# Kernel tuning notes

Hardware: AMD Instinct MI355X
Metric: run time of the kernel (lower is better)

Reference implementation:

```python
import jax, jax.numpy as jnp
import numpy as np

C = 1.2            # PoincareBall curvature (learnable in torch, init value used)
SQC = C ** 0.5
MIN_NORM = 1e-15
BALL_EPS = 4e-3    # geoopt float32 projx eps

def _artanh(x):
    return jnp.arctanh(jnp.clip(x, -1.0 + 1e-7, 1.0 - 1e-7))

def _tanh(x):
    return jnp.tanh(jnp.clip(x, -15.0, 15.0))

def _norm(x):
    return jnp.maximum(jnp.linalg.norm(x, axis=-1, keepdims=True), MIN_NORM)

def p_projx(x):
    n = _norm(x)
    maxnorm = (1.0 - BALL_EPS) / SQC
    return jnp.where(n > maxnorm, x / n * maxnorm, x)

def p_expmap0(u):
    n = _norm(u)
    return p_projx(_tanh(SQC * n) * u / (SQC * n))

def p_logmap0(y):
    n = _norm(y)
    return _artanh(SQC * n) * y / (SQC * n)

def p_mobius_add(x, y):
    x2 = jnp.sum(x * x, -1, keepdims=True)
    y2 = jnp.sum(y * y, -1, keepdims=True)
    xy = jnp.sum(x * y, -1, keepdims=True)
    num = (1 + 2 * C * xy + C * y2) * x + (1 - C * x2) * y
    den = 1 + 2 * C * xy + C * C * x2 * y2
    return num / jnp.maximum(den, MIN_NORM)

def p_mobius_matvec(W, x):
    xn = _norm(x)
    mx = x @ W.T
    mxn = _norm(mx)
    res = _tanh(mxn / xn * _artanh(SQC * xn)) * mx / (mxn * SQC)
    zero = jnp.all(mx == 0, axis=-1, keepdims=True)
    return p_projx(jnp.where(zero, jnp.zeros_like(res), res))

def p_mobius_scalar_mul(r, x):
    n = _norm(x)
    return p_projx(_tanh(r * _artanh(SQC * n)) * x / (n * SQC))

def p_linear(x, W, b):
    # Manifold_Linear on PoincareBall: mobius matvec + mobius bias add + projx
    mv = p_mobius_matvec(W, x)
    return p_projx(p_mobius_add(mv, p_expmap0(b)))

def e_linear(x, W, b):
    return x @ W.T + b

def mob_relu(x):
    # Mob_Act: logmap0 -> act -> expmap0 (with projection)
    return p_expmap0(jax.nn.relu(p_logmap0(x)))


def setup_inputs() -> dict:
    key = jax.random.key(0)
    ks = jax.random.split(key, 26)
    g = lambda i, shape, s: (jax.random.normal(ks[i], shape, jnp.float32) * s)
    d = {
        'x':   g(0, (1024, 32, 128), 1.0),
        'We1': g(1, (80, 32), 0.1),   'be1': g(2, (80,), 0.05),
        'We2': g(3, (104, 80), 0.1),  'be2': g(4, (104,), 0.05),
        'We3': g(5, (128, 104), 0.1), 'be3': g(6, (128,), 0.05),
        'Wh1': g(7, (80, 32), 0.1),   'bh1': g(8, (80,), 0.05),
        'Wh2': g(9, (104, 80), 0.1),  'bh2': g(10, (104,), 0.05),
        'Wh3': g(11, (128, 104), 0.1),'bh3': g(12, (128,), 0.05),
        'Wae': g(13, (128, 128), 0.1),'bae': g(14, (128,), 0.05),
        'Wah': g(15, (128, 128), 0.1),'bah': g(16, (128,), 0.05),
        'Wte': g(17, (1, 128), 0.1),  'bte': g(18, (1,), 0.05),
        'Wth': g(19, (1, 128), 0.1),  'bth': g(20, (1,), 0.05),
        'Wf1': g(21, (10, 256), 0.1), 'bf1': g(22, (10,), 0.05),
        'Wf2': g(23, (10, 10), 0.1),  'bf2': g(24, (10,), 0.05),
    }
    return d


def reference(x, We1, be1, We2, be2, We3, be3,
              Wh1, bh1, Wh2, bh2, Wh3, bh3,
              Wae, bae, Wah, bah, Wte, bte, Wth, bth,
              Wf1, bf1, Wf2, bf2):
    xs = jnp.transpose(x, (0, 2, 1))  # (B, S, C_in)

    # --- Euclidean branch: expmap0 = identity; Manifold_Linear = plain linear ---
    xe = xs
    xe = e_linear(xe, We1, be1); xe = jax.nn.relu(xe)
    xe = e_linear(xe, We2, be2); xe = jax.nn.relu(xe)
    xe = e_linear(xe, We3, be3)
    out_e = jax.nn.relu(xe)               # extra self.act for Euclidean manifolds

    # --- Poincare branch ---
    xh = p_expmap0(xs)
    xh = p_linear(xh, Wh1, bh1); xh = mob_relu(xh)
    xh = p_linear(xh, Wh2, bh2); xh = mob_relu(xh)
    out_h = p_linear(xh, Wh3, bh3)        # (B, S, part_dim)

    # --- cross-manifold attention in tangent space at origin ---
    tan_e = e_linear(out_e, Wae, bae)                    # Euclidean logmap0 = id
    tan_h = p_logmap0(p_linear(out_h, Wah, bah))
    mu = 0.5 * (tan_e + tan_h)
    a_e = e_linear(tan_e - mu, Wte, bte)  # (B, S, 1)
    a_h = e_linear(tan_h - mu, Wth, bth)
    w = jax.nn.softmax(jnp.stack([a_e, a_h], axis=0), axis=0)
    proc_e = w[0] * out_e                                # Euclidean mobius scalar mul
    proc_h = p_mobius_scalar_mul(w[1], out_h)

    # --- pool over constituents in tangent space, concat, classify ---
    o_e = jnp.mean(proc_e, axis=1)                       # Euclidean logmap0 = id
    o_h = jnp.mean(p_logmap0(proc_h), axis=1)
    o = jnp.concatenate([o_e, o_h], axis=-1)             # (B, 2*part_dim)
    o = jax.nn.relu(e_linear(o, Wf1, bf1))
    return e_linear(o, Wf2, bf2)
```

## Files before the change

kernel.cpp:

```cpp
#include <hip/hip_runtime.h>
#include <math.h>

constexpr float CC   = 1.2f;
constexpr float SQC  = 1.09544511501033215f;
constexpr float MAXN = (1.0f - 4e-3f) / SQC;
constexpr float MINN = 1e-15f;

constexpr int WTH1 = 0;
constexpr int WTH2 = 4096;
constexpr int WTH3 = 14336;
constexpr int WTAH = 27648;
constexpr int WTE1 = 44032;
constexpr int WTE2 = 48128;
constexpr int WTE3 = 58368;
constexpr int EB1  = 71680;
constexpr int EB2  = 71808;
constexpr int EB3  = 71936;
constexpr int EBA  = 72064;
constexpr int BE1  = 72192;
constexpr int BE2  = 72320;
constexpr int BE3  = 72448;
constexpr int U1o  = 72576;
constexpr int U2o  = 72704;
constexpr int SCo  = 72832;

constexpr int ASTR  = 129;
constexpr int L_ACT = 0;
constexpr int L_ZH  = 16512;
constexpr int L_SCR = 17792;
constexpr int L_F1  = 19328;
constexpr int L_TOT = 19344;

__device__ __forceinline__ float art_(float x){
  x = fminf(fmaxf(x, -0.9999999f), 0.9999999f);
  return 0.5f * __logf((1.0f + x) / (1.0f - x));
}
__device__ __forceinline__ float tanh_(float x){
  x = fminf(fmaxf(x, -15.0f), 15.0f);
  float e = __expf(2.0f * x);
  return (e - 1.0f) / (e + 1.0f);
}
__device__ __forceinline__ float wsum(float v){
#pragma unroll
  for(int i=32;i>0;i>>=1) v += __shfl_xor(v, i, 64);
  return v;
}
__device__ __forceinline__ float rtj(float v){
  v += __shfl_xor(v, 1, 64); v += __shfl_xor(v, 2, 64);
  v += __shfl_xor(v, 4, 64); v += __shfl_xor(v, 8, 64);
  return v;
}
__device__ __forceinline__ float lamv(float nv){
  float n = fmaxf(nv, MINN);
  return art_(SQC*n)/(SQC*n);
}
struct HS { float ca, cb, nv; };
__device__ __forceinline__ HS hyper_chain(float m2, float meb, float xn_in, float y2){
  float xn  = fmaxf(xn_in, MINN);
  float mxn = fmaxf(sqrtf(m2), MINN);
  float r   = art_(SQC*xn);
  float s   = tanh_(mxn/xn*r)/(mxn*SQC);
  float nr  = s*mxn;
  if(nr > MAXN){ s *= MAXN/nr; nr = MAXN; }
  float xy = s*meb, x2 = nr*nr;
  float den = fmaxf(1.f + 2.f*CC*xy + CC*CC*x2*y2, MINN);
  float A   = (1.f + 2.f*CC*xy + CC*y2)/den;
  float Bc  = (1.f - CC*x2)/den;
  float n3  = sqrtf(fmaxf(A*A*x2 + 2.f*A*Bc*xy + Bc*Bc*y2, 0.f));
  float rho = (n3 > MAXN) ? MAXN/n3 : 1.f;
  HS h; h.nv = fminf(n3, MAXN); h.ca = rho*A*s; h.cb = rho*Bc;
  return h;
}
struct TT { float tau, nf; };
__device__ __forceinline__ TT tail_relu(float rn2){
  float rn = fmaxf(sqrtf(rn2), MINN);
  float th = tanh_(SQC*rn);
  TT r; r.tau = th/(SQC*rn); r.nf = th/SQC;
  if(r.nf > MAXN){ r.tau *= MAXN/r.nf; r.nf = MAXN; }
  return r;
}
struct EX { float nh, scl; };
__device__ __forceinline__ EX exp0(float n2){
  float n0 = fmaxf(sqrtf(n2), MINN);
  float th = tanh_(SQC*n0);
  EX e; e.nh = th/SQC; e.scl = th/(SQC*n0);
  if(e.nh > MAXN){ e.scl *= MAXN/e.nh; e.nh = MAXN; }
  return e;
}
struct THW { float te, th2; };
__device__ __forceinline__ THW ahchain(float m2a, float mw1, float mw2, float meba,
                                       float xnh, float rr, float y2,
                                       float ebw1, float ebw2){
  float mxn = fmaxf(sqrtf(m2a), MINN);
  float s = tanh_(mxn/xnh*rr)/(mxn*SQC);
  float nr = s*mxn;
  if(nr > MAXN){ s *= MAXN/nr; nr = MAXN; }
  float xy = s*meba, x2 = nr*nr;
  float den = fmaxf(1.f + 2.f*CC*xy + CC*CC*x2*y2, MINN);
  float A = (1.f + 2.f*CC*xy + CC*y2)/den;
  float Bc = (1.f - CC*x2)/den;
  float n3 = sqrtf(fmaxf(A*A*x2 + 2.f*A*Bc*xy + Bc*Bc*y2, 0.f));
  float rho = (n3 > MAXN) ? MAXN/n3 : 1.f;
  float nv = fminf(n3, MAXN);
  float lr = lamv(nv)*rho;
  THW r; r.te = lr*(A*s*mw1 + Bc*ebw1); r.th2 = lr*(A*s*mw2 + Bc*ebw2);
  return r;
}
struct AG { float wge, g2; };
__device__ __forceinline__ AG attn(float d1, float d2, float thte, float thth,
                                   float rr, float xnh, float b_e, float b_h){
  float a_e = 0.5f*(d1 - thte) + b_e;
  float a_h = 0.5f*(thth - d2) + b_h;
  float mx = fmaxf(a_e, a_h);
  float ee = __expf(a_e - mx), eh = __expf(a_h - mx);
  float inv = 1.f/(ee + eh);
  AG r; r.wge = ee*inv;
  float wgh = eh*inv;
  float inner = wgh*rr;
  float scl2 = tanh_(inner)/(xnh*SQC);
  float nn = scl2*xnh;
  if(nn > MAXN){ scl2 *= MAXN/nn; nn = MAXN; }
  r.g2 = lamv(nn)*scl2;
  return r;
}

__global__ void k_setup_a(const float* __restrict__ Wae, const float* __restrict__ bae,
                          const float* __restrict__ bh1, const float* __restrict__ bh2,
                          const float* __restrict__ bh3, const float* __restrict__ bah,
                          const float* __restrict__ Wte, const float* __restrict__ Wth,
                          const float* __restrict__ be1, const float* __restrict__ be2,
                          const float* __restrict__ be3, float* __restrict__ ws){
  const int tid = threadIdx.x;
  {
    const int which = tid >> 7, k = tid & 127;
    const float* wv = which ? Wth : Wte;
    float s = 0.f;
#pragma unroll 4
    for(int j=0;j<128;++j) s += Wae[j*128+k] * wv[j];
    ws[(which ? U2o : U1o) + k] = s;
  }
  if(tid < 128){
    ws[BE1+tid] = (tid < 80)  ? be1[tid] : 0.f;
    ws[BE2+tid] = (tid < 104) ? be2[tid] : 0.f;
    ws[BE3+tid] = be3[tid];
  }
  if(tid < 64){
    const int l = tid;
    float p1=0.f, p2=0.f;
    for(int j=l;j<128;j+=64){ p1 += bae[j]*Wte[j]; p2 += bae[j]*Wth[j]; }
    p1 = wsum(p1); p2 = wsum(p2);
    if(l==0){ ws[SCo+0]=p1; ws[SCo+1]=p2; }
    const float* bs[4] = {bh1,bh2,bh3,bah};
    const int dims[4]  = {80,104,128,128};
    const int offs[4]  = {EB1,EB2,EB3,EBA};
    for(int v=0;v<4;++v){
      const float* bp = bs[v]; const int D = dims[v];
      float q = 0.f;
      for(int j=l;j<D;j+=64) q += bp[j]*bp[j];
      q = wsum(q);
      float nb = fmaxf(sqrtf(q), MINN);
      float th = tanhf(fminf(fmaxf(SQC*nb,-15.f),15.f));
      float coef = th/(SQC*nb);
      float ne = th/SQC;
      if(ne > MAXN){ coef *= MAXN/ne; ne = MAXN; }
      for(int j=l;j<D;j+=64) ws[offs[v]+j] = coef*bp[j];
      for(int j=D+l;j<128;j+=64) ws[offs[v]+j] = 0.f;
      if(l==0) ws[SCo+2+v] = ne*ne;
      if(v==3){
        float e1=0.f, e2=0.f;
        for(int j=l;j<D;j+=64){ e1 += bp[j]*Wte[j]; e2 += bp[j]*Wth[j]; }
        e1 = wsum(e1)*coef; e2 = wsum(e2)*coef;
        if(l==0){ ws[SCo+6]=e1; ws[SCo+7]=e2; }
      }
    }
  }
}

__global__ void k_trans(const float* __restrict__ Wh1, const float* __restrict__ Wh2,
                        const float* __restrict__ Wh3, const float* __restrict__ Wah,
                        const float* __restrict__ We1, const float* __restrict__ We2,
                        const float* __restrict__ We3, float* __restrict__ ws){
  const int blk = blockIdx.x, j = threadIdx.x;
  const float* W; int OUT, K, kk, dst;
  if(blk < 32)       { W=Wh1; OUT=80;  K=32;  kk=blk;      dst=WTH1; }
  else if(blk < 112) { W=Wh2; OUT=104; K=80;  kk=blk-32;   dst=WTH2; }
  else if(blk < 216) { W=Wh3; OUT=128; K=104; kk=blk-112;  dst=WTH3; }
  else if(blk < 344) { W=Wah; OUT=128; K=128; kk=blk-216;  dst=WTAH; }
  else if(blk < 376) { W=We1; OUT=80;  K=32;  kk=blk-344;  dst=WTE1; }
  else if(blk < 456) { W=We2; OUT=104; K=80;  kk=blk-376;  dst=WTE2; }
  else               { W=We3; OUT=128; K=104; kk=blk-456;  dst=WTE3; }
  ws[dst + kk*128 + j] = (j < OUT) ? W[j*K + kk] : 0.f;
}

__device__ __forceinline__ void ld8(const float* __restrict__ p, float (&v)[8]){
  float4 a = *(const float4*)p, b = *(const float4*)(p+4);
  v[0]=a.x; v[1]=a.y; v[2]=a.z; v[3]=a.w; v[4]=b.x; v[5]=b.y; v[6]=b.z; v[7]=b.w;
}

template<int K, bool XG, bool XSQ>
__device__ __forceinline__ void gemm(const float* __restrict__ wt,
                                     const float* __restrict__ xg,
                                     const float* __restrict__ ACT,
                                     int tj, int tt, float (&acc)[8][8], float (&xsq)[8]){
#pragma unroll
  for(int i=0;i<8;++i)
#pragma unroll
    for(int j=0;j<8;++j) acc[i][j] = 0.f;
  const int wo = tj*8, xo = tt*8;
#pragma unroll 4
  for(int k=0;k<K;++k){
    float4 w0 = *(const float4*)(wt + k*128 + wo);
    float4 w1 = *(const float4*)(wt + k*128 + wo + 4);
    float4 xa, xb;
    if(XG){ xa = *(const float4*)(xg + k*128 + xo); xb = *(const float4*)(xg + k*128 + xo + 4); }
    else  { xa = *(const float4*)(ACT + k*ASTR + xo); xb = *(const float4*)(ACT + k*ASTR + xo + 4); }
    float xv[8] = {xa.x,xa.y,xa.z,xa.w,xb.x,xb.y,xb.z,xb.w};
    float wv[8] = {w0.x,w0.y,w0.z,w0.w,w1.x,w1.y,w1.z,w1.w};
#pragma unroll
    for(int i=0;i<8;++i){
      if(XSQ) xsq[i] = fmaf(xv[i], xv[i], xsq[i]);
#pragma unroll
      for(int j=0;j<8;++j) acc[i][j] = fmaf(xv[i], wv[j], acc[i][j]);
    }
  }
}

__device__ __forceinline__ void wACT(float* __restrict__ ACT, const float (&acc)[8][8],
                                     int tj, int tt){
#pragma unroll
  for(int j=0;j<8;++j){
    float4 a = {acc[0][j],acc[1][j],acc[2][j],acc[3][j]};
    float4 b = {acc[4][j],acc[5][j],acc[6][j],acc[7][j]};
    float* p = ACT + (tj*8+j)*ASTR + tt*8;
    *(float4*)p = a; *(float4*)(p+4) = b;
  }
}

__global__ __launch_bounds__(256, 2) void k_main(
    const float* __restrict__ x,
    const float* __restrict__ Wf1, const float* __restrict__ bf1,
    const float* __restrict__ Wf2, const float* __restrict__ bf2,
    const float* __restrict__ Wte, const float* __restrict__ bte,
    const float* __restrict__ Wth, const float* __restrict__ bth,
    const float* __restrict__ ws, float* __restrict__ out){
  extern __shared__ float lds[];
  float* ACT = lds + L_ACT;
  float* ZH  = lds + L_ZH;
  float* SCR = lds + L_SCR;
  float* F1V = lds + L_F1;
  const int tid = threadIdx.x, tj = tid & 15, tt = tid >> 4, b = blockIdx.x;
  const int tok0 = tt*8;
  const bool isTok = tid < 128;
  const float* xb = x + (size_t)b*4096;

  float acc[8][8];
  float xsq[8];
#pragma unroll
  for(int i=0;i<8;++i) xsq[i] = 0.f;

  float nf = 0.f, rr = 0.f, xnh = 1.f, thte = 0.f, thth = 0.f;

  {
    gemm<32,true,true>(ws+WTH1, xb, ACT, tj, tt, acc, xsq);
    float ebv[8]; ld8(ws+EB1+tj*8, ebv);
#pragma unroll
    for(int i=0;i<8;++i){
      float s=0.f, e=0.f;
#pragma unroll
      for(int j=0;j<8;++j){ s = fmaf(acc[i][j],acc[i][j],s); e = fmaf(acc[i][j],ebv[j],e); }
      s = rtj(s); e = rtj(e);
      if(tj==0){ SCR[tok0+i]=s; SCR[128+tok0+i]=e; SCR[256+tok0+i]=xsq[i]; }
    }
    __syncthreads();
    if(isTok){
      EX e0 = exp0(SCR[256+tid]);
      float scl0 = e0.scl;
      float m2 = SCR[tid]*scl0*scl0, meb = SCR[128+tid]*scl0;
      HS h = hyper_chain(m2, meb, e0.nh, ws[SCo+2]);
      SCR[tid] = h.ca*scl0; SCR[128+tid] = h.cb; SCR[256+tid] = lamv(h.nv);
    }
    __syncthreads();
    float cav[8],cbv[8],lmv[8];
#pragma unroll
    for(int i=0;i<8;++i){ cav[i]=SCR[tok0+i]; cbv[i]=SCR[128+tok0+i]; lmv[i]=SCR[256+tok0+i]; }
#pragma unroll
    for(int i=0;i<8;++i){
      float s=0.f;
#pragma unroll
      for(int j=0;j<8;++j){
        float v = fmaxf(lmv[i]*fmaf(cav[i],acc[i][j],cbv[i]*ebv[j]), 0.f);
        acc[i][j]=v; s = fmaf(v,v,s);
      }
      s = rtj(s);
      if(tj==0) SCR[384+tok0+i]=s;
    }
    __syncthreads();
    if(isTok){ TT tr = tail_relu(SCR[384+tid]); nf = tr.nf; SCR[384+tid]=tr.tau; }
    __syncthreads();
#pragma unroll
    for(int i=0;i<8;++i){ float tau=SCR[384+tok0+i];
#pragma unroll
      for(int j=0;j<8;++j) acc[i][j]*=tau; }
    wACT(ACT, acc, tj, tt);
    __syncthreads();
  }

  {
    gemm<80,false,false>(ws+WTH2, nullptr, ACT, tj, tt, acc, xsq);
    float ebv[8]; ld8(ws+EB2+tj*8, ebv);
#pragma unroll
    for(int i=0;i<8;++i){
      float s=0.f, e=0.f;
#pragma unroll
      for(int j=0;j<8;++j){ s = fmaf(acc[i][j],acc[i][j],s); e = fmaf(acc[i][j],ebv[j],e); }
      s = rtj(s); e = rtj(e);
      if(tj==0){ SCR[tok0+i]=s; SCR[128+tok0+i]=e; }
    }
    __syncthreads();
    if(isTok){
      HS h = hyper_chain(SCR[tid], SCR[128+tid], nf, ws[SCo+3]);
      SCR[tid]=h.ca; SCR[128+tid]=h.cb; SCR[256+tid]=lamv(h.nv);
    }
    __syncthreads();
    float cav[8],cbv[8],lmv[8];
#pragma unroll
    for(int i=0;i<8;++i){ cav[i]=SCR[tok0+i]; cbv[i]=SCR[128+tok0+i]; lmv[i]=SCR[256+tok0+i]; }
#pragma unroll
    for(int i=0;i<8;++i){
      float s=0.f;
#pragma unroll
      for(int j=0;j<8;++j){
        float v = fmaxf(lmv[i]*fmaf(cav[i],acc[i][j],cbv[i]*ebv[j]), 0.f);
        acc[i][j]=v; s = fmaf(v,v,s);
      }
      s = rtj(s);
      if(tj==0) SCR[384+tok0+i]=s;
    }
    __syncthreads();
    if(isTok){ TT tr = tail_relu(SCR[384+tid]); nf = tr.nf; SCR[384+tid]=tr.tau; }
    __syncthreads();
#pragma unroll
    for(int i=0;i<8;++i){ float tau=SCR[384+tok0+i];
#pragma unroll
      for(int j=0;j<8;++j) acc[i][j]*=tau; }
    wACT(ACT, acc, tj, tt);
    __syncthreads();
  }

  {
    gemm<104,false,false>(ws+WTH3, nullptr, ACT, tj, tt, acc, xsq);
    float ebv[8]; ld8(ws+EB3+tj*8, ebv);
#pragma unroll
    for(int i=0;i<8;++i){
      float s=0.f, e=0.f;
#pragma unroll
      for(int j=0;j<8;++j){ s = fmaf(acc[i][j],acc[i][j],s); e = fmaf(acc[i][j],ebv[j],e); }
      s = rtj(s); e = rtj(e);
      if(tj==0){ SCR[tok0+i]=s; SCR[128+tok0+i]=e; }
    }
    __syncthreads();
    if(isTok){
      HS h = hyper_chain(SCR[tid], SCR[128+tid], nf, ws[SCo+4]);
      xnh = fmaxf(h.nv, MINN);
      rr  = art_(SQC*xnh);
      SCR[tid]=h.ca; SCR[128+tid]=h.cb;
    }
    __syncthreads();
    float cav[8],cbv[8];
#pragma unroll
    for(int i=0;i<8;++i){ cav[i]=SCR[tok0+i]; cbv[i]=SCR[128+tok0+i]; }
#pragma unroll
    for(int i=0;i<8;++i)
#pragma unroll
      for(int j=0;j<8;++j) acc[i][j] = fmaf(cav[i],acc[i][j],cbv[i]*ebv[j]);
    wACT(ACT, acc, tj, tt);
#pragma unroll
    for(int ic=0;ic<10;++ic){
      float wf[8]; ld8(Wf1 + ic*256 + 128 + tj*8, wf);
#pragma unroll
      for(int i=0;i<8;++i){
        float s=0.f;
#pragma unroll
        for(int j=0;j<8;++j) s = fmaf(acc[i][j], wf[j], s);
        s = rtj(s);
        if(tj==0) ZH[ic*128 + tok0 + i] = s;
      }
    }
    __syncthreads();
  }

  {
    gemm<128,false,false>(ws+WTAH, nullptr, ACT, tj, tt, acc, xsq);
    float w1v[8], w2v[8], eav[8];
    ld8(Wte + tj*8, w1v); ld8(Wth + tj*8, w2v); ld8(ws+EBA+tj*8, eav);
#pragma unroll
    for(int i=0;i<8;++i){
      float s0=0.f,s1=0.f,s2=0.f,s3=0.f;
#pragma unroll
      for(int j=0;j<8;++j){
        float m = acc[i][j];
        s0 = fmaf(m,m,s0); s1 = fmaf(m,w1v[j],s1);
        s2 = fmaf(m,w2v[j],s2); s3 = fmaf(m,eav[j],s3);
      }
      s0=rtj(s0); s1=rtj(s1); s2=rtj(s2); s3=rtj(s3);
      if(tj==0){ SCR[tok0+i]=s0; SCR[128+tok0+i]=s1; SCR[256+tok0+i]=s2; SCR[384+tok0+i]=s3; }
    }
    __syncthreads();
    if(isTok){
      THW a = ahchain(SCR[tid], SCR[128+tid], SCR[256+tid], SCR[384+tid],
                      xnh, rr, ws[SCo+5], ws[SCo+6], ws[SCo+7]);
      thte = a.te; thth = a.th2;
    }
  }

  {
    gemm<32,true,false>(ws+WTE1, xb, ACT, tj, tt, acc, xsq);
    float bev[8]; ld8(ws+BE1+tj*8, bev);
#pragma unroll
    for(int i=0;i<8;++i)
#pragma unroll
      for(int j=0;j<8;++j) acc[i][j] = fmaxf(acc[i][j]+bev[j], 0.f);
    wACT(ACT, acc, tj, tt);
    __syncthreads();
  }
  {
    gemm<80,false,false>(ws+WTE2, nullptr, ACT, tj, tt, acc, xsq);
    float bev[8]; ld8(ws+BE2+tj*8, bev);
#pragma unroll
    for(int i=0;i<8;++i)
#pragma unroll
      for(int j=0;j<8;++j) acc[i][j] = fmaxf(acc[i][j]+bev[j], 0.f);
    __syncthreads();
    wACT(ACT, acc, tj, tt);
    __syncthreads();
  }
  {
    gemm<104,false,false>(ws+WTE3, nullptr, ACT, tj, tt, acc, xsq);
    float bev[8], u1v[8], u2v[8];
    ld8(ws+BE3+tj*8, bev); ld8(ws+U1o+tj*8, u1v); ld8(ws+U2o+tj*8, u2v);
#pragma unroll
    for(int i=0;i<8;++i){
      float s1=0.f, s2=0.f;
#pragma unroll
      for(int j=0;j<8;++j){
        float v = fmaxf(acc[i][j]+bev[j], 0.f);
        acc[i][j] = v;
        s1 = fmaf(v,u1v[j],s1); s2 = fmaf(v,u2v[j],s2);
      }
      s1=rtj(s1); s2=rtj(s2);
      if(tj==0){ SCR[tok0+i]=s1; SCR[128+tok0+i]=s2; }
    }
#pragma unroll
    for(int ic=0;ic<10;++ic){
      float wf[8]; ld8(Wf1 + ic*256 + tj*8, wf);
#pragma unroll
      for(int i=0;i<8;++i){
        float s=0.f;
#pragma unroll
        for(int j=0;j<8;++j) s = fmaf(acc[i][j], wf[j], s);
        s = rtj(s);
        if(tj==0) SCR[(2+ic)*128 + tok0 + i] = s;
      }
    }
    __syncthreads();
    if(isTok){
      float d1 = SCR[tid] + ws[SCo+0];
      float d2 = SCR[128+tid] + ws[SCo+1];
      AG g = attn(d1, d2, thte, thth, rr, xnh, bte[0], bth[0]);
#pragma unroll
      for(int ic=0;ic<10;++ic){
        float p = fmaf(g.wge, SCR[(2+ic)*128+tid], g.g2 * ZH[ic*128+tid]);
        SCR[(2+ic)*128+tid] = p;
      }
    }
    __syncthreads();
    if(tid < 10){
      float s = 0.f;
      const float* P = SCR + (2+tid)*128;
      for(int t2=0;t2<128;++t2) s += P[t2];
      F1V[tid] = fmaxf(s*(1.f/128.f) + bf1[tid], 0.f);
    }
    __syncthreads();
    if(tid < 10){
      float o = bf2[tid];
#pragma unroll
      for(int k2=0;k2<10;++k2) o = fmaf(Wf2[tid*10+k2], F1V[k2], o);
      out[b*10 + tid] = o;
    }
  }
}

extern "C" void kernel_launch(void* const* d_in, const int* in_sizes, int n_in,
                              void* d_out, int out_size, void* d_ws, size_t ws_size,
                              hipStream_t stream){
  (void)in_sizes; (void)n_in; (void)out_size; (void)ws_size;
  const float* x   = (const float*)d_in[0];
  const float* We1 = (const float*)d_in[1];
  const float* be1 = (const float*)d_in[2];
  const float* We2 = (const float*)d_in[3];
  const float* be2 = (const float*)d_in[4];
  const float* We3 = (const float*)d_in[5];
  const float* be3 = (const float*)d_in[6];
  const float* Wh1 = (const float*)d_in[7];
  const float* bh1 = (const float*)d_in[8];
  const float* Wh2 = (const float*)d_in[9];
  const float* bh2 = (const float*)d_in[10];
  const float* Wh3 = (const float*)d_in[11];
  const float* bh3 = (const float*)d_in[12];
  const float* Wae = (const float*)d_in[13];
  const float* bae = (const float*)d_in[14];
  const float* Wah = (const float*)d_in[15];
  const float* bah = (const float*)d_in[16];
  const float* Wte = (const float*)d_in[17];
  const float* bte = (const float*)d_in[18];
  const float* Wth = (const float*)d_in[19];
  const float* bth = (const float*)d_in[20];
  const float* Wf1 = (const float*)d_in[21];
  const float* bf1 = (const float*)d_in[22];
  const float* Wf2 = (const float*)d_in[23];
  const float* bf2 = (const float*)d_in[24];
  float* ws  = (float*)d_ws;
  float* out = (float*)d_out;

  hipLaunchKernelGGL(k_setup_a, dim3(1), dim3(256), 0, stream,
                     Wae, bae, bh1, bh2, bh3, bah, Wte, Wth, be1, be2, be3, ws);
  hipLaunchKernelGGL(k_trans, dim3(560), dim3(128), 0, stream,
                     Wh1, Wh2, Wh3, Wah, We1, We2, We3, ws);

  const int smem = L_TOT * 4;
  hipFuncSetAttribute((const void*)k_main,
                      hipFuncAttributeMaxDynamicSharedMemorySize, smem);
  hipLaunchKernelGGL(k_main, dim3(1024), dim3(256), smem, stream,
                     x, Wf1, bf1, Wf2, bf2, Wte, bte, Wth, bth, ws, out);
}
```

Before: 620.9 us.

## Split each batch row across two blocks and finish pooling in a separate kernel

Each batch row's 128 tokens are now split across two blocks of 64 tokens each. Each thread now computes a 4x8 register tile instead of 8x8, and the launch bound rises to 4 blocks per CU. Each block writes its per-row partial sums for the 10 pooled features to workspace, and a new small kernel k_fin combines the two halves and applies the final ReLU and Wf2 layer. The aim is more parallelism and occupancy from a smaller LDS footprint and fewer registers, at the cost of a second launch, a global round trip for the partials, and less reuse per register tile.

```diff
diff --git a/kernel.cpp b/kernel.cpp
--- a/kernel.cpp
+++ b/kernel.cpp
@@ -23,13 +23,13 @@
 constexpr int U1o  = 72576;
 constexpr int U2o  = 72704;
 constexpr int SCo  = 72832;
-
-constexpr int ASTR  = 129;
+constexpr int PART = 72864;
+
+constexpr int ASTR  = 65;
 constexpr int L_ACT = 0;
-constexpr int L_ZH  = 16512;
-constexpr int L_SCR = 17792;
-constexpr int L_F1  = 19328;
-constexpr int L_TOT = 19344;
+constexpr int L_ZH  = 8320;
+constexpr int L_SCR = 8960;
+constexpr int L_TOT = 9728;
 
 __device__ __forceinline__ float art_(float x){
   x = fminf(fmaxf(x, -0.9999999f), 0.9999999f);
@@ -192,32 +192,50 @@
   ws[dst + kk*128 + j] = (j < OUT) ? W[j*K + kk] : 0.f;
 }
 
+__global__ void k_fin(const float* __restrict__ ws, const float* __restrict__ bf1,
+                      const float* __restrict__ Wf2, const float* __restrict__ bf2,
+                      float* __restrict__ out){
+  const int r = blockIdx.x*64 + threadIdx.x;
+  const float* p = ws + PART + (size_t)r*20;
+  float f1[10];
+#pragma unroll
+  for(int i=0;i<10;++i)
+    f1[i] = fmaxf((p[i] + p[10+i])*(1.f/128.f) + bf1[i], 0.f);
+#pragma unroll
+  for(int o=0;o<10;++o){
+    float a = bf2[o];
+#pragma unroll
+    for(int k=0;k<10;++k) a = fmaf(Wf2[o*10+k], f1[k], a);
+    out[r*10 + o] = a;
+  }
+}
+
 __device__ __forceinline__ void ld8(const float* __restrict__ p, float (&v)[8]){
   float4 a = *(const float4*)p, b = *(const float4*)(p+4);
   v[0]=a.x; v[1]=a.y; v[2]=a.z; v[3]=a.w; v[4]=b.x; v[5]=b.y; v[6]=b.z; v[7]=b.w;
 }
 
 template<int K, bool XG, bool XSQ>
-__device__ __forceinline__ void gemm(const float* __restrict__ wt,
-                                     const float* __restrict__ xg,
-                                     const float* __restrict__ ACT,
-                                     int tj, int tt, float (&acc)[8][8], float (&xsq)[8]){
-#pragma unroll
-  for(int i=0;i<8;++i)
+__device__ __forceinline__ void gemm4(const float* __restrict__ wt,
+                                      const float* __restrict__ xg,
+                                      const float* __restrict__ ACT,
+                                      int tj, int tt, float (&acc)[4][8], float (&xsq)[4]){
+#pragma unroll
+  for(int i=0;i<4;++i)
 #pragma unroll
     for(int j=0;j<8;++j) acc[i][j] = 0.f;
-  const int wo = tj*8, xo = tt*8;
+  const int wo = tj*8, xo = tt*4;
 #pragma unroll 4
   for(int k=0;k<K;++k){
     float4 w0 = *(const float4*)(wt + k*128 + wo);
     float4 w1 = *(const float4*)(wt + k*128 + wo + 4);
-    float4 xa, xb;
-    if(XG){ xa = *(const float4*)(xg + k*128 + xo); xb = *(const float4*)(xg + k*128 + xo + 4); }
-    else  { xa = *(const float4*)(ACT + k*ASTR + xo); xb = *(const float4*)(ACT + k*ASTR + xo + 4); }
-    float xv[8] = {xa.x,xa.y,xa.z,xa.w,xb.x,xb.y,xb.z,xb.w};
+    float4 xa;
+    if(XG) xa = *(const float4*)(xg + k*128 + xo);
+    else   xa = *(const float4*)(ACT + k*ASTR + xo);
+    float xv[4] = {xa.x,xa.y,xa.z,xa.w};
     float wv[8] = {w0.x,w0.y,w0.z,w0.w,w1.x,w1.y,w1.z,w1.w};
 #pragma unroll
-    for(int i=0;i<8;++i){
+    for(int i=0;i<4;++i){
       if(XSQ) xsq[i] = fmaf(xv[i], xv[i], xsq[i]);
 #pragma unroll
       for(int j=0;j<8;++j) acc[i][j] = fmaf(xv[i], wv[j], acc[i][j]);
@@ -225,66 +243,62 @@
   }
 }
 
-__device__ __forceinline__ void wACT(float* __restrict__ ACT, const float (&acc)[8][8],
+__device__ __forceinline__ void wACT(float* __restrict__ ACT, const float (&acc)[4][8],
                                      int tj, int tt){
 #pragma unroll
   for(int j=0;j<8;++j){
     float4 a = {acc[0][j],acc[1][j],acc[2][j],acc[3][j]};
-    float4 b = {acc[4][j],acc[5][j],acc[6][j],acc[7][j]};
-    float* p = ACT + (tj*8+j)*ASTR + tt*8;
-    *(float4*)p = a; *(float4*)(p+4) = b;
-  }
-}
-
-__global__ __launch_bounds__(256, 2) void k_main(
+    *(float4*)(ACT + (tj*8+j)*ASTR + tt*4) = a;
+  }
+}
+
+__global__ __launch_bounds__(256, 4) void k_main(
     const float* __restrict__ x,
-    const float* __restrict__ Wf1, const float* __restrict__ bf1,
-    const float* __restrict__ Wf2, const float* __restrict__ bf2,
-    const float* __restrict__ Wte, const float* __restrict__ bte,
-    const float* __restrict__ Wth, const float* __restrict__ bth,
-    const float* __restrict__ ws, float* __restrict__ out){
+    const float* __restrict__ Wf1, const float* __restrict__ Wte,
+    const float* __restrict__ bte, const float* __restrict__ Wth,
+    const float* __restrict__ bth, float* __restrict__ ws){
   extern __shared__ float lds[];
   float* ACT = lds + L_ACT;
   float* ZH  = lds + L_ZH;
   float* SCR = lds + L_SCR;
-  float* F1V = lds + L_F1;
-  const int tid = threadIdx.x, tj = tid & 15, tt = tid >> 4, b = blockIdx.x;
-  const int tok0 = tt*8;
-  const bool isTok = tid < 128;
-  const float* xb = x + (size_t)b*4096;
-
-  float acc[8][8];
-  float xsq[8];
-#pragma unroll
-  for(int i=0;i<8;++i) xsq[i] = 0.f;
+  const int tid = threadIdx.x, tj = tid & 15, tt = tid >> 4;
+  const int b = blockIdx.x, b2 = b >> 1, hf = b & 1;
+  const int tok0 = tt*4;
+  const bool isTok = tid < 64;
+  const float* xg = x + (size_t)b2*4096 + hf*64;
+
+  float acc[4][8];
+  float xsq[4];
+#pragma unroll
+  for(int i=0;i<4;++i) xsq[i] = 0.f;
 
   float nf = 0.f, rr = 0.f, xnh = 1.f, thte = 0.f, thth = 0.f;
 
   {
-    gemm<32,true,true>(ws+WTH1, xb, ACT, tj, tt, acc, xsq);
+    gemm4<32,true,true>(ws+WTH1, xg, ACT, tj, tt, acc, xsq);
     float ebv[8]; ld8(ws+EB1+tj*8, ebv);
 #pragma unroll
-    for(int i=0;i<8;++i){
+    for(int i=0;i<4;++i){
       float s=0.f, e=0.f;
 #pragma unroll
       for(int j=0;j<8;++j){ s = fmaf(acc[i][j],acc[i][j],s); e = fmaf(acc[i][j],ebv[j],e); }
       s = rtj(s); e = rtj(e);
-      if(tj==0){ SCR[tok0+i]=s; SCR[128+tok0+i]=e; SCR[256+tok0+i]=xsq[i]; }
+      if(tj==0){ SCR[tok0+i]=s; SCR[64+tok0+i]=e; SCR[128+tok0+i]=xsq[i]; }
     }
     __syncthreads();
     if(isTok){
-      EX e0 = exp0(SCR[256+tid]);
+      EX e0 = exp0(SCR[128+tid]);
       float scl0 = e0.scl;
-      float m2 = SCR[tid]*scl0*scl0, meb = SCR[128+tid]*scl0;
+      float m2 = SCR[tid]*scl0*scl0, meb = SCR[64+tid]*scl0;
       HS h = hyper_chain(m2, meb, e0.nh, ws[SCo+2]);
-      SCR[tid] = h.ca*scl0; SCR[128+tid] = h.cb; SCR[256+tid] = lamv(h.nv);
-    }
-    __syncthreads();
-    float cav[8],cbv[8],lmv[8];
-#pragma unroll
-    for(int i=0;i<8;++i){ cav[i]=SCR[tok0+i]; cbv[i]=SCR[128+tok0+i]; lmv[i]=SCR[256+tok0+i]; }
-#pragma unroll
-    for(int i=0;i<8;++i){
+      SCR[tid] = h.ca*scl0; SCR[64+tid] = h.cb; SCR[128+tid] = lamv(h.nv);
+    }
+    __syncthreads();
+    float cav[4],cbv[4],lmv[4];
+#pragma unroll
+    for(int i=0;i<4;++i){ cav[i]=SCR[tok0+i]; cbv[i]=SCR[64+tok0+i]; lmv[i]=SCR[128+tok0+i]; }
+#pragma unroll
+    for(int i=0;i<4;++i){
       float s=0.f;
 #pragma unroll
       for(int j=0;j<8;++j){
@@ -292,13 +306,13 @@
         acc[i][j]=v; s = fmaf(v,v,s);
       }
       s = rtj(s);
-      if(tj==0) SCR[384+tok0+i]=s;
-    }
-    __syncthreads();
-    if(isTok){ TT tr = tail_relu(SCR[384+tid]); nf = tr.nf; SCR[384+tid]=tr.tau; }
-    __syncthreads();
-#pragma unroll
-    for(int i=0;i<8;++i){ float tau=SCR[384+tok0+i];
+      if(tj==0) SCR[192+tok0+i]=s;
+    }
+    __syncthreads();
+    if(isTok){ TT tr = tail_relu(SCR[192+tid]); nf = tr.nf; SCR[192+tid]=tr.tau; }
+    __syncthreads();
+#pragma unroll
+    for(int i=0;i<4;++i){ float tau=SCR[192+tok0+i];
 #pragma unroll
       for(int j=0;j<8;++j) acc[i][j]*=tau; }
     wACT(ACT, acc, tj, tt);
@@ -306,27 +320,27 @@
   }
 
   {
-    gemm<80,false,false>(ws+WTH2, nullptr, ACT, tj, tt, acc, xsq);
+    gemm4<80,false,false>(ws+WTH2, nullptr, ACT, tj, tt, acc, xsq);
     float ebv[8]; ld8(ws+EB2+tj*8, ebv);
 #pragma unroll
-    for(int i=0;i<8;++i){
+    for(int i=0;i<4;++i){
       float s=0.f, e=0.f;
 #pragma unroll
       for(int j=0;j<8;++j){ s = fmaf(acc[i][j],acc[i][j],s); e = fmaf(acc[i][j],ebv[j],e); }
       s = rtj(s); e = rtj(e);
-      if(tj==0){ SCR[tok0+i]=s; SCR[128+tok0+i]=e; }
+      if(tj==0){ SCR[tok0+i]=s; SCR[64+tok0+i]=e; }
     }
     __syncthreads();
     if(isTok){
-      HS h = hyper_chain(SCR[tid], SCR[128+tid], nf, ws[SCo+3]);
-      SCR[tid]=h.ca; SCR[128+tid]=h.cb; SCR[256+tid]=lamv(h.nv);
-    }
-    __syncthreads();
-    float cav[8],cbv[8],lmv[8];
-#pragma unroll
-    for(int i=0;i<8;++i){ cav[i]=SCR[tok0+i]; cbv[i]=SCR[128+tok0+i]; lmv[i]=SCR[256+tok0+i]; }
-#pragma unroll
-    for(int i=0;i<8;++i){
+      HS h = hyper_chain(SCR[tid], SCR[64+tid], nf, ws[SCo+3]);
+      SCR[tid]=h.ca; SCR[64+tid]=h.cb; SCR[128+tid]=lamv(h.nv);
+    }
+    __syncthreads();
+    float cav[4],cbv[4],lmv[4];
+#pragma unroll
+    for(int i=0;i<4;++i){ cav[i]=SCR[tok0+i]; cbv[i]=SCR[64+tok0+i]; lmv[i]=SCR[128+tok0+i]; }
+#pragma unroll
+    for(int i=0;i<4;++i){
       float s=0.f;
 #pragma unroll
       for(int j=0;j<8;++j){
@@ -334,13 +348,13 @@
         acc[i][j]=v; s = fmaf(v,v,s);
       }
       s = rtj(s);
-      if(tj==0) SCR[384+tok0+i]=s;
-    }
-    __syncthreads();
-    if(isTok){ TT tr = tail_relu(SCR[384+tid]); nf = tr.nf; SCR[384+tid]=tr.tau; }
-    __syncthreads();
-#pragma unroll
-    for(int i=0;i<8;++i){ float tau=SCR[384+tok0+i];
+      if(tj==0) SCR[192+tok0+i]=s;
+    }
+    __syncthreads();
+    if(isTok){ TT tr = tail_relu(SCR[192+tid]); nf = tr.nf; SCR[192+tid]=tr.tau; }
+    __syncthreads();
+#pragma unroll
+    for(int i=0;i<4;++i){ float tau=SCR[192+tok0+i];
 #pragma unroll
       for(int j=0;j<8;++j) acc[i][j]*=tau; }
     wACT(ACT, acc, tj, tt);
@@ -348,29 +362,29 @@
   }
 
   {
-    gemm<104,false,false>(ws+WTH3, nullptr, ACT, tj, tt, acc, xsq);
+    gemm4<104,false,false>(ws+WTH3, nullptr, ACT, tj, tt, acc, xsq);
     float ebv[8]; ld8(ws+EB3+tj*8, ebv);
 #pragma unroll
-    for(int i=0;i<8;++i){
+    for(int i=0;i<4;++i){
       float s=0.f, e=0.f;
 #pragma unroll
       for(int j=0;j<8;++j){ s = fmaf(acc[i][j],acc[i][j],s); e = fmaf(acc[i][j],ebv[j],e); }
       s = rtj(s); e = rtj(e);
-      if(tj==0){ SCR[tok0+i]=s; SCR[128+tok0+i]=e; }
+      if(tj==0){ SCR[tok0+i]=s; SCR[64+tok0+i]=e; }
     }
     __syncthreads();
     if(isTok){
-      HS h = hyper_chain(SCR[tid], SCR[128+tid], nf, ws[SCo+4]);
+      HS h = hyper_chain(SCR[tid], SCR[64+tid], nf, ws[SCo+4]);
       xnh = fmaxf(h.nv, MINN);
       rr  = art_(SQC*xnh);
-      SCR[tid]=h.ca; SCR[128+tid]=h.cb;
-    }
-    __syncthreads();
-    float cav[8],cbv[8];
-#pragma unroll
-    for(int i=0;i<8;++i){ cav[i]=SCR[tok0+i]; cbv[i]=SCR[128+tok0+i]; }
-#pragma unroll
-    for(int i=0;i<8;++i)
+      SCR[tid]=h.ca; SCR[64+tid]=h.cb;
+    }
+    __syncthreads();
+    float cav[4],cbv[4];
+#pragma unroll
+    for(int i=0;i<4;++i){ cav[i]=SCR[tok0+i]; cbv[i]=SCR[64+tok0+i]; }
+#pragma unroll
+    for(int i=0;i<4;++i)
 #pragma unroll
       for(int j=0;j<8;++j) acc[i][j] = fmaf(cav[i],acc[i][j],cbv[i]*ebv[j]);
     wACT(ACT, acc, tj, tt);
@@ -378,23 +392,23 @@
     for(int ic=0;ic<10;++ic){
       float wf[8]; ld8(Wf1 + ic*256 + 128 + tj*8, wf);
 #pragma unroll
-      for(int i=0;i<8;++i){
+      for(int i=0;i<4;++i){
         float s=0.f;
 #pragma unroll
         for(int j=0;j<8;++j) s = fmaf(acc[i][j], wf[j], s);
         s = rtj(s);
-        if(tj==0) ZH[ic*128 + tok0 + i] = s;
-      }
-    }
-    __syncthreads();
-  }
-
-  {
-    gemm<128,false,false>(ws+WTAH, nullptr, ACT, tj, tt, acc, xsq);
+        if(tj==0) ZH[ic*64 + tok0 + i] = s;
+      }
+    }
+    __syncthreads();
+  }
+
+  {
+    gemm4<128,false,false>(ws+WTAH, nullptr, ACT, tj, tt, acc, xsq);
     float w1v[8], w2v[8], eav[8];
     ld8(Wte + tj*8, w1v); ld8(Wth + tj*8, w2v); ld8(ws+EBA+tj*8, eav);
 #pragma unroll
-    for(int i=0;i<8;++i){
+    for(int i=0;i<4;++i){
       float s0=0.f,s1=0.f,s2=0.f,s3=0.f;
 #pragma unroll
       for(int j=0;j<8;++j){
@@ -403,31 +417,32 @@
         s2 = fmaf(m,w2v[j],s2); s3 = fmaf(m,eav[j],s3);
       }
       s0=rtj(s0); s1=rtj(s1); s2=rtj(s2); s3=rtj(s3);
-      if(tj==0){ SCR[tok0+i]=s0; SCR[128+tok0+i]=s1; SCR[256+tok0+i]=s2; SCR[384+tok0+i]=s3; }
+      if(tj==0){ SCR[tok0+i]=s0; SCR[64+tok0+i]=s1; SCR[128+tok0+i]=s2; SCR[192+tok0+i]=s3; }
     }
     __syncthreads();
     if(isTok){
-      THW a = ahchain(SCR[tid], SCR[128+tid], SCR[256+tid], SCR[384+tid],
+      THW a = ahchain(SCR[tid], SCR[64+tid], SCR[128+tid], SCR[192+tid],
                       xnh, rr, ws[SCo+5], ws[SCo+6], ws[SCo+7]);
       thte = a.te; thth = a.th2;
     }
   }
 
   {
-    gemm<32,true,false>(ws+WTE1, xb, ACT, tj, tt, acc, xsq);
+    gemm4<32,true,false>(ws+WTE1, xg, ACT, tj, tt, acc, xsq);
     float bev[8]; ld8(ws+BE1+tj*8, bev);
 #pragma unroll
-    for(int i=0;i<8;++i)
+    for(int i=0;i<4;++i)
 #pragma unroll
       for(int j=0;j<8;++j) acc[i][j] = fmaxf(acc[i][j]+bev[j], 0.f);
+    __syncthreads();
     wACT(ACT, acc, tj, tt);
     __syncthreads();
   }
   {
-    gemm<80,false,false>(ws+WTE2, nullptr, ACT, tj, tt, acc, xsq);
+    gemm4<80,false,false>(ws+WTE2, nullptr, ACT, tj, tt, acc, xsq);
     float bev[8]; ld8(ws+BE2+tj*8, bev);
 #pragma unroll
-    for(int i=0;i<8;++i)
+    for(int i=0;i<4;++i)
 #pragma unroll
       for(int j=0;j<8;++j) acc[i][j] = fmaxf(acc[i][j]+bev[j], 0.f);
     __syncthreads();
@@ -435,11 +450,11 @@
     __syncthreads();
   }
   {
-    gemm<104,false,false>(ws+WTE3, nullptr, ACT, tj, tt, acc, xsq);
+    gemm4<104,false,false>(ws+WTE3, nullptr, ACT, tj, tt, acc, xsq);
     float bev[8], u1v[8], u2v[8];
     ld8(ws+BE3+tj*8, bev); ld8(ws+U1o+tj*8, u1v); ld8(ws+U2o+tj*8, u2v);
 #pragma unroll
-    for(int i=0;i<8;++i){
+    for(int i=0;i<4;++i){
       float s1=0.f, s2=0.f;
 #pragma unroll
       for(int j=0;j<8;++j){
@@ -448,44 +463,35 @@
         s1 = fmaf(v,u1v[j],s1); s2 = fmaf(v,u2v[j],s2);
       }
       s1=rtj(s1); s2=rtj(s2);
-      if(tj==0){ SCR[tok0+i]=s1; SCR[128+tok0+i]=s2; }
+      if(tj==0){ SCR[tok0+i]=s1; SCR[64+tok0+i]=s2; }
     }
 #pragma unroll
     for(int ic=0;ic<10;++ic){
       float wf[8]; ld8(Wf1 + ic*256 + tj*8, wf);
 #pragma unroll
-      for(int i=0;i<8;++i){
+      for(int i=0;i<4;++i){
         float s=0.f;
 #pragma unroll
         for(int j=0;j<8;++j) s = fmaf(acc[i][j], wf[j], s);
         s = rtj(s);
-        if(tj==0) SCR[(2+ic)*128 + tok0 + i] = s;
+        if(tj==0) SCR[(2+ic)*64 + tok0 + i] = s;
       }
     }
     __syncthreads();
     if(isTok){
       float d1 = SCR[tid] + ws[SCo+0];
-      float d2 = SCR[128+tid] + ws[SCo+1];
+      float d2 = SCR[64+tid] + ws[SCo+1];
       AG g = attn(d1, d2, thte, thth, rr, xnh, bte[0], bth[0]);
+      float pv[10];
 #pragma unroll
       for(int ic=0;ic<10;++ic){
-        float p = fmaf(g.wge, SCR[(2+ic)*128+tid], g.g2 * ZH[ic*128+tid]);
-        SCR[(2+ic)*128+tid] = p;
-      }
-    }
-    __syncthreads();
-    if(tid < 10){
-      float s = 0.f;
-      const float* P = SCR + (2+tid)*128;
-      for(int t2=0;t2<128;++t2) s += P[t2];
-      F1V[tid] = fmaxf(s*(1.f/128.f) + bf1[tid], 0.f);
-    }
-    __syncthreads();
-    if(tid < 10){
-      float o = bf2[tid];
-#pragma unroll
-      for(int k2=0;k2<10;++k2) o = fmaf(Wf2[tid*10+k2], F1V[k2], o);
-      out[b*10 + tid] = o;
+        float p = fmaf(g.wge, SCR[(2+ic)*64+tid], g.g2 * ZH[ic*64+tid]);
+        pv[ic] = wsum(p);
+      }
+      if(tid == 0){
+#pragma unroll
+        for(int ic=0;ic<10;++ic) ws[PART + (size_t)b*10 + ic] = pv[ic];
+      }
     }
   }
 }
@@ -528,8 +534,9 @@
                      Wh1, Wh2, Wh3, Wah, We1, We2, We3, ws);
 
   const int smem = L_TOT * 4;
-  hipFuncSetAttribute((const void*)k_main,
-                      hipFuncAttributeMaxDynamicSharedMemorySize, smem);
-  hipLaunchKernelGGL(k_main, dim3(1024), dim3(256), smem, stream,
-                     x, Wf1, bf1, Wf2, bf2, Wte, bte, Wth, bth, ws, out);
-}
+  hipLaunchKernelGGL(k_main, dim3(2048), dim3(256), smem, stream,
+                     x, Wf1, Wte, bte, Wth, bth, ws);
+
+  hipLaunchKernelGGL(k_fin, dim3(16), dim3(64), 0, stream,
+                     ws, bf1, Wf2, bf2, out);
+}
```

Result: faster. 572.5 us (-7.8%).
